# Kernel tuning notes

Measured on AMD Instinct MI355X. Metric: run time of the kernel, lower is better.

Reference implementation:

```python
import jax, jax.numpy as jnp
import numpy as np

B, S, E = 2, 2048, 1024
H, KVH, D = 16, 4, 64
ROPE_BASE = 10000.0


def setup_inputs() -> dict:
    key = jax.random.key(0)
    ks = jax.random.split(key, 7)
    s = 0.02
    return {
        "query_inputs": jax.random.normal(ks[0], (B, S, E), jnp.float32),
        "key_inputs": jax.random.normal(ks[1], (B, S, E), jnp.float32),
        "value_inputs": jax.random.normal(ks[2], (B, S, E), jnp.float32),
        "attention_mask": jnp.ones((1, 1, S, S), dtype=bool),
        "Wq": jax.random.normal(ks[3], (E, H * D), jnp.float32) * s,
        "Wk": jax.random.normal(ks[4], (E, KVH * D), jnp.float32) * s,
        "Wv": jax.random.normal(ks[5], (E, KVH * D), jnp.float32) * s,
        "Wo": jax.random.normal(ks[6], (H * D, E), jnp.float32) * s,
    }


def _rotate_half(x):
    x1, x2 = jnp.split(x, 2, axis=-1)
    return jnp.concatenate((-x2, x1), axis=-1)


def _rope(k, q):
    # standard RoPE, rescaling_factor=None -> base 10000
    d = q.shape[-1]
    inv_freq = 1.0 / (ROPE_BASE ** (jnp.arange(0, d, 2, dtype=jnp.float32) / d))
    t = jnp.arange(q.shape[1], dtype=jnp.float32)
    freqs = jnp.einsum("i,j->ij", t, inv_freq)          # [S, d/2]
    emb = jnp.concatenate((freqs, freqs), axis=-1)       # [S, d]
    cos = jnp.cos(emb)[None, :, None, :]                 # [1, S, 1, d]
    sin = jnp.sin(emb)[None, :, None, :]
    apply = lambda x: x * cos + _rotate_half(x) * sin
    return apply(k), apply(q)


def reference(query_inputs, key_inputs, value_inputs, attention_mask, Wq, Wk, Wv, Wo):
    q = (query_inputs @ Wq).reshape(B, S, H, D)
    k = (key_inputs @ Wk).reshape(B, S, KVH, D)
    v = (value_inputs @ Wv).reshape(B, S, KVH, D)
    k, q = _rope(k, q)
    n_rep = H // KVH
    k = jnp.repeat(k, n_rep, axis=2)                     # [B, S, H, D]
    v = jnp.repeat(v, n_rep, axis=2)
    logits = jnp.einsum("bthd,bThd->bhtT", q, k) / jnp.sqrt(jnp.float32(D))
    logits = jnp.where(attention_mask, logits, jnp.float32(-1e30))
    w = jax.nn.softmax(logits, axis=-1)                  # [B, H, S, S]
    out = jnp.einsum("bhtT,bThd->bthd", w, v).reshape(B, S, H * D)
    return out @ Wo
```

## Files before the change

kernel.cpp:

```cpp
#include <hip/hip_runtime.h>
#include <hip/hip_bf16.h>
#include <math.h>

#define Bsz 2
#define Sseq 2048
#define Edim 1024
#define Hq 16
#define KVH 4
#define Dh 64

typedef __attribute__((ext_vector_type(4))) float f32x4;
typedef __attribute__((ext_vector_type(16))) float f32x16;
typedef __attribute__((ext_vector_type(8))) short bf16x8;

__device__ inline unsigned short f2bf(float f) {
    union { float f; unsigned int u; } v; v.f = f;
    unsigned int u = v.u;
    u += 0x7FFFu + ((u >> 16) & 1u);
    return (unsigned short)(u >> 16);
}

__device__ inline unsigned int cvt_pk_bf16(float a, float b) {
    unsigned int r;
    asm("v_cvt_pk_bf16_f32 %0, %1, %2" : "=v"(r) : "v"(a), "v"(b));
    return r;
}

__device__ inline f32x4 mfma16(bf16x8 a, bf16x8 b, f32x4 c) {
    return __builtin_amdgcn_mfma_f32_16x16x32_bf16(a, b, c, 0, 0, 0);
}

__device__ inline f32x16 mfma32(bf16x8 a, bf16x8 b, f32x16 c) {
    return __builtin_amdgcn_mfma_f32_32x32x16_bf16(a, b, c, 0, 0, 0);
}

__device__ inline void gload_lds16(const void* g, void* l) {
    __builtin_amdgcn_global_load_lds(
        (const __attribute__((address_space(1))) unsigned int*)g,
        (__attribute__((address_space(3))) unsigned int*)l, 16, 0, 0);
}

__global__ __launch_bounds__(256)
void prep(const float* __restrict__ Xq, const float* __restrict__ Xk,
          const float* __restrict__ Xv,
          const float* __restrict__ Wq, const float* __restrict__ Wk,
          const float* __restrict__ Wv, const float* __restrict__ Wo,
          unsigned short* __restrict__ Xq_b, unsigned short* __restrict__ Xk_b,
          unsigned short* __restrict__ Xv_b,
          unsigned short* __restrict__ Wq_t, unsigned short* __restrict__ Wk_t,
          unsigned short* __restrict__ Wv_t, unsigned short* __restrict__ Wo_t,
          float* __restrict__ tab) {
    int bid = blockIdx.x;
    if (bid < 256) {
        int idx = bid * 256 + threadIdx.x;
        int s = idx >> 5, j = idx & 31;
        double inv = pow(10000.0, -(double)(2 * j) / 64.0);
        double a = (double)s * inv;
        tab[idx * 2 + 0] = (float)cos(a);
        tab[idx * 2 + 1] = (float)sin(a);
        return;
    }
    bid -= 256;
    if (bid < 12288) {
        const float* X; unsigned short* Y;
        if (bid < 4096)      { X = Xq; Y = Xq_b; }
        else if (bid < 8192) { X = Xk; Y = Xk_b; bid -= 4096; }
        else                 { X = Xv; Y = Xv_b; bid -= 8192; }
        int i = bid * 256 + threadIdx.x;
        float4 v = ((const float4*)X)[i];
        ushort4 o;
        o.x = f2bf(v.x); o.y = f2bf(v.y); o.z = f2bf(v.z); o.w = f2bf(v.w);
        ((ushort4*)Y)[i] = o;
        return;
    }
    bid -= 12288;
    const float* W; unsigned short* Wt; int N; int local;
    if (bid < 1024)      { W = Wq; Wt = Wq_t; N = 1024; local = bid; }
    else if (bid < 1280) { W = Wk; Wt = Wk_t; N = 256;  local = bid - 1024; }
    else if (bid < 1536) { W = Wv; Wt = Wv_t; N = 256;  local = bid - 1280; }
    else                 { W = Wo; Wt = Wo_t; N = 1024; local = bid - 1536; }
    __shared__ float tile[32][33];
    int nb = N >> 5;
    int bn = (local % nb) * 32, bk = (local / nb) * 32;
    int tx = threadIdx.x & 31, ty = threadIdx.x >> 5;
    #pragma unroll
    for (int i = 0; i < 32; i += 8)
        tile[ty + i][tx] = W[(size_t)(bk + ty + i) * N + bn + tx];
    __syncthreads();
    #pragma unroll
    for (int i = 0; i < 32; i += 8)
        Wt[(size_t)(bn + ty + i) * 1024 + bk + tx] = f2bf(tile[tx][ty + i]);
}

__global__ __launch_bounds__(256)
void qkv_gemm(const unsigned short* __restrict__ Xq_b,
              const unsigned short* __restrict__ Xk_b,
              const unsigned short* __restrict__ Xv_b,
              const unsigned short* __restrict__ Wq_t,
              const unsigned short* __restrict__ Wk_t,
              const unsigned short* __restrict__ Wv_t,
              unsigned short* __restrict__ Qb,
              unsigned short* __restrict__ Kbf,
              unsigned short* __restrict__ Vt,
              const float* __restrict__ tab, float qscale) {
    __shared__ __attribute__((aligned(16))) unsigned short Alds[128 * 64];
    __shared__ __attribute__((aligned(16))) unsigned short Blds[128 * 64];

    int bid = blockIdx.x;
    const unsigned short *A, *Bt;
    unsigned short* C;
    int m0, n0, N, epi;
    float prescale;
    if (bid < 256) {
        A = Xq_b; Bt = Wq_t; C = Qb;
        m0 = (bid & 31) << 7; n0 = (bid >> 5) << 7; N = 1024; epi = 0; prescale = qscale;
    } else if (bid < 320) {
        int l = bid - 256;
        A = Xk_b; Bt = Wk_t; C = Kbf;
        m0 = (l & 31) << 7; n0 = (l >> 5) << 7; N = 256; epi = 0; prescale = 1.f;
    } else {
        int l = bid - 320;
        A = Xv_b; Bt = Wv_t; C = Vt;
        m0 = (l & 31) << 7; n0 = (l >> 5) << 7; N = 256; epi = 1; prescale = 1.f;
    }

    const int t = threadIdx.x;
    const int wid = t >> 6, lane = t & 63;
    const int l15 = lane & 15, l4 = lane >> 4;
    const int wm = (wid >> 1) * 64, wn = (wid & 1) * 64;

    f32x4 acc[4][4] = {};

    for (int k0 = 0; k0 < 1024; k0 += 64) {
        #pragma unroll
        for (int i = 0; i < 4; ++i) {
            int slot = t + 256 * i;
            int row = slot >> 3, ch = slot & 7;
            int g = ch ^ (row & 7);
            gload_lds16(A + (size_t)(m0 + row) * 1024 + k0 + g * 8, &Alds[slot * 8]);
            gload_lds16(Bt + (size_t)(n0 + row) * 1024 + k0 + g * 8, &Blds[slot * 8]);
        }
        __syncthreads();
        __builtin_amdgcn_s_setprio(1);
        #pragma unroll
        for (int kc = 0; kc < 2; ++kc) {
            bf16x8 af[4], bfr[4];
            #pragma unroll
            for (int mt = 0; mt < 4; ++mt)
                af[mt] = *(const bf16x8*)&Alds[(wm + mt * 16 + l15) * 64 + (((kc * 4 + l4) ^ (l15 & 7)) * 8)];
            #pragma unroll
            for (int nt = 0; nt < 4; ++nt)
                bfr[nt] = *(const bf16x8*)&Blds[(wn + nt * 16 + l15) * 64 + (((kc * 4 + l4) ^ (l15 & 7)) * 8)];
            #pragma unroll
            for (int mt = 0; mt < 4; ++mt)
                #pragma unroll
                for (int nt = 0; nt < 4; ++nt)
                    acc[mt][nt] = mfma16(af[mt], bfr[nt], acc[mt][nt]);
        }
        __builtin_amdgcn_s_setprio(0);
        __syncthreads();
    }

    if (epi == 0) {
        #pragma unroll
        for (int mt = 0; mt < 4; ++mt) {
            int rbase = m0 + wm + mt * 16 + 4 * l4;
            #pragma unroll
            for (int nt = 0; nt < 2; ++nt) {
                int col = n0 + wn + nt * 16 + l15;
                int j = col & 31;
                #pragma unroll
                for (int r = 0; r < 4; ++r) {
                    int row = rbase + r;
                    int s = row & (Sseq - 1);
                    float c = tab[(s * 32 + j) * 2 + 0];
                    float sn = tab[(s * 32 + j) * 2 + 1];
                    float x1 = acc[mt][nt][r] * prescale;
                    float x2 = acc[mt][nt + 2][r] * prescale;
                    C[(size_t)row * N + col]      = f2bf(x1 * c - x2 * sn);
                    C[(size_t)row * N + col + 32] = f2bf(x2 * c + x1 * sn);
                }
            }
        }
    } else {
        #pragma unroll
        for (int mt = 0; mt < 4; ++mt)
            #pragma unroll
            for (int nt = 0; nt < 4; ++nt)
                #pragma unroll
                for (int r = 0; r < 4; ++r) {
                    int row = m0 + wm + mt * 16 + 4 * l4 + r;
                    int col = n0 + wn + nt * 16 + l15;
                    int b = row >> 11, s = row & (Sseq - 1);
                    C[((size_t)(b * 256 + col) << 11) + s] = f2bf(acc[mt][nt][r]);
                }
    }
}

__global__ __launch_bounds__(256)
void wo_gemm(const unsigned short* __restrict__ A,
             const unsigned short* __restrict__ Bt,
             float* __restrict__ C) {
    __shared__ __attribute__((aligned(16))) unsigned short Alds[128 * 64];
    __shared__ __attribute__((aligned(16))) unsigned short Blds[128 * 64];
    const int t = threadIdx.x;
    const int wid = t >> 6, lane = t & 63;
    const int l15 = lane & 15, l4 = lane >> 4;
    const int m0 = blockIdx.x * 128, n0 = blockIdx.y * 128;
    const int wm = (wid >> 1) * 64, wn = (wid & 1) * 64;

    f32x4 acc[4][4] = {};

    for (int k0 = 0; k0 < 1024; k0 += 64) {
        #pragma unroll
        for (int i = 0; i < 4; ++i) {
            int slot = t + 256 * i;
            int row = slot >> 3, ch = slot & 7;
            int g = ch ^ (row & 7);
            gload_lds16(A + (size_t)(m0 + row) * 1024 + k0 + g * 8, &Alds[slot * 8]);
            gload_lds16(Bt + (size_t)(n0 + row) * 1024 + k0 + g * 8, &Blds[slot * 8]);
        }
        __syncthreads();
        __builtin_amdgcn_s_setprio(1);
        #pragma unroll
        for (int kc = 0; kc < 2; ++kc) {
            bf16x8 af[4], bfr[4];
            #pragma unroll
            for (int mt = 0; mt < 4; ++mt)
                af[mt] = *(const bf16x8*)&Alds[(wm + mt * 16 + l15) * 64 + (((kc * 4 + l4) ^ (l15 & 7)) * 8)];
            #pragma unroll
            for (int nt = 0; nt < 4; ++nt)
                bfr[nt] = *(const bf16x8*)&Blds[(wn + nt * 16 + l15) * 64 + (((kc * 4 + l4) ^ (l15 & 7)) * 8)];
            #pragma unroll
            for (int mt = 0; mt < 4; ++mt)
                #pragma unroll
                for (int nt = 0; nt < 4; ++nt)
                    acc[mt][nt] = mfma16(af[mt], bfr[nt], acc[mt][nt]);
        }
        __builtin_amdgcn_s_setprio(0);
        __syncthreads();
    }

    #pragma unroll
    for (int mt = 0; mt < 4; ++mt)
        #pragma unroll
        for (int nt = 0; nt < 4; ++nt)
            #pragma unroll
            for (int r = 0; r < 4; ++r)
                C[(size_t)(m0 + wm + mt * 16 + 4 * l4 + r) * 1024 + n0 + wn + nt * 16 + l15]
                    = acc[mt][nt][r];
}

__global__ __launch_bounds__(128)
void attn(const unsigned short* __restrict__ Q,
          const unsigned short* __restrict__ Kb,
          const unsigned short* __restrict__ Vt,
          unsigned short* __restrict__ O) {
    __shared__ __attribute__((aligned(16))) unsigned short Klds[2][64 * 64];
    __shared__ __attribute__((aligned(16))) unsigned short Vlds[2][64 * 64];

    const int t = threadIdx.x, wid = t >> 6, lane = t & 63;
    const int l31 = lane & 31, hi = lane >> 5;
    const int q0 = blockIdx.x * 64;
    const int bh = blockIdx.y;
    const int b = bh >> 4, h = bh & 15, kvh = h >> 2;
    const int qb0 = (b << 11) + q0 + wid * 32;

    bf16x8 qf[4];
    {
        const unsigned short* qp = Q + (size_t)(qb0 + l31) * 1024 + h * 64 + hi * 8;
        #pragma unroll
        for (int kc = 0; kc < 4; ++kc)
            qf[kc] = *(const bf16x8*)(qp + kc * 16);
    }

    f32x16 accO[2] = {};
    float lrow = 0.f;

    #define STAGE(buf, kt)                                                              \
        do {                                                                            \
            int kbase = (kt) * 64;                                                      \
            _Pragma("unroll")                                                           \
            for (int i = 0; i < 4; ++i) {                                               \
                int slot = t + 128 * i;                                                 \
                int row = slot >> 3, ch = slot & 7;                                     \
                int g = ch ^ (row & 7);                                                 \
                gload_lds16(Kb + ((size_t)((b << 11) + kbase + row) << 8) + kvh * 64 + g * 8, \
                            &Klds[buf][slot * 8]);                                      \
                gload_lds16(Vt + ((size_t)((b * 4 + kvh) * 64 + row) << 11) + kbase + g * 8,  \
                            &Vlds[buf][slot * 8]);                                      \
            }                                                                           \
        } while (0)

    STAGE(0, 0);
    asm volatile("s_waitcnt vmcnt(0)");
    __syncthreads();

    int cur = 0;
    for (int kt = 0; kt < Sseq / 64; ++kt) {
        if (kt + 1 < Sseq / 64) STAGE(cur ^ 1, kt + 1);

        f32x16 sacc[2] = {};
        __builtin_amdgcn_s_setprio(1);
        #pragma unroll
        for (int kc = 0; kc < 4; ++kc) {
            #pragma unroll
            for (int kb = 0; kb < 2; ++kb) {
                int row = kb * 32 + l31;
                bf16x8 kf = *(const bf16x8*)
                    &Klds[cur][row * 64 + (((kc * 2 + hi) ^ (row & 7)) * 8)];
                sacc[kb] = mfma32(kf, qf[kc], sacc[kb]);
            }
        }
        __builtin_amdgcn_s_setprio(0);

        float pv[2][16];
        float rs = 0.f;
        #pragma unroll
        for (int kb = 0; kb < 2; ++kb)
            #pragma unroll
            for (int r = 0; r < 16; ++r) {
                float p = __builtin_amdgcn_exp2f(sacc[kb][r]);
                pv[kb][r] = p;
                rs += p;
            }
        lrow += rs + __shfl_xor(rs, 32);

        bf16x8 pa[4];
        #pragma unroll
        for (int kb = 0; kb < 2; ++kb) {
            #pragma unroll
            for (int half = 0; half < 2; ++half) {
                const float* p = &pv[kb][half * 8];
                unsigned int u0 = cvt_pk_bf16(p[0], p[1]);
                unsigned int u1 = cvt_pk_bf16(p[2], p[3]);
                unsigned int u2 = cvt_pk_bf16(p[4], p[5]);
                unsigned int u3 = cvt_pk_bf16(p[6], p[7]);
                asm("v_permlane32_swap_b32 %0, %1" : "+v"(u0), "+v"(u2));
                asm("v_permlane32_swap_b32 %0, %1" : "+v"(u1), "+v"(u3));
                uint4 w; w.x = u0; w.y = u1; w.z = u2; w.w = u3;
                pa[kb * 2 + half] = *(bf16x8*)&w;
            }
        }

        __builtin_amdgcn_s_setprio(1);
        #pragma unroll
        for (int kq = 0; kq < 4; ++kq) {
            #pragma unroll
            for (int db = 0; db < 2; ++db) {
                int row = db * 32 + l31;
                bf16x8 vf = *(const bf16x8*)
                    &Vlds[cur][row * 64 + (((kq * 2 + hi) ^ (row & 7)) * 8)];
                accO[db] = mfma32(pa[kq], vf, accO[db]);
            }
        }
        __builtin_amdgcn_s_setprio(0);

        asm volatile("s_waitcnt vmcnt(0)");
        __syncthreads();
        cur ^= 1;
    }
    #undef STAGE

    float linv = __builtin_amdgcn_rcpf(lrow);
    #pragma unroll
    for (int r = 0; r < 16; ++r) {
        int q = (r & 3) + 8 * (r >> 2) + 4 * hi;
        float li = __shfl(linv, q);
        #pragma unroll
        for (int db = 0; db < 2; ++db) {
            int col = h * 64 + db * 32 + l31;
            O[(size_t)(qb0 + q) * 1024 + col] = f2bf(accO[db][r] * li);
        }
    }
}

extern "C" void kernel_launch(void* const* d_in, const int* in_sizes, int n_in,
                              void* d_out, int out_size, void* d_ws, size_t ws_size,
                              hipStream_t stream) {
    const float* Xq = (const float*)d_in[0];
    const float* Xk = (const float*)d_in[1];
    const float* Xv = (const float*)d_in[2];
    const float* Wq = (const float*)d_in[4];
    const float* Wk = (const float*)d_in[5];
    const float* Wv = (const float*)d_in[6];
    const float* Wo = (const float*)d_in[7];

    char* ws = (char*)d_ws;
    unsigned short* Xq_b = (unsigned short*)(ws + 0);
    unsigned short* Xk_b = (unsigned short*)(ws + 8388608);
    unsigned short* Xv_b = (unsigned short*)(ws + 16777216);
    unsigned short* Qb   = (unsigned short*)(ws + 25165824);
    unsigned short* Kbf  = (unsigned short*)(ws + 33554432);
    unsigned short* Vt   = (unsigned short*)(ws + 35651584);
    unsigned short* AttO = (unsigned short*)(ws + 37748736);
    unsigned short* Wq_t = (unsigned short*)(ws + 46137344);
    unsigned short* Wk_t = (unsigned short*)(ws + 48234496);
    unsigned short* Wv_t = (unsigned short*)(ws + 48758784);
    unsigned short* Wo_t = (unsigned short*)(ws + 49283072);
    float*          tab  = (float*)(ws + 51380224);

    prep<<<dim3(15104), 256, 0, stream>>>(Xq, Xk, Xv, Wq, Wk, Wv, Wo,
                                          Xq_b, Xk_b, Xv_b,
                                          Wq_t, Wk_t, Wv_t, Wo_t, tab);

    const float qscale = 0.125f * 1.44269504088896340736f;
    qkv_gemm<<<dim3(384), 256, 0, stream>>>(Xq_b, Xk_b, Xv_b, Wq_t, Wk_t, Wv_t,
                                            Qb, Kbf, Vt, tab, qscale);

    attn<<<dim3(32, 32), 128, 0, stream>>>(Qb, Kbf, Vt, AttO);

    wo_gemm<<<dim3(32, 8), 256, 0, stream>>>(AttO, Wo_t, (float*)d_out);
}
```

Baseline: 115.9 us.

## Split attention over key halves with separate combine kernel

The attention kernel now uses 256-thread blocks covering 128 queries and splits the key sequence into two halves across grid z, writing unnormalized-per-half outputs and row sums to workspace. A new combine kernel reweights the two partial outputs by their row sums and writes the final bf16 attention output. This doubles the grid size and shares each K/V tile between four waves, trading an extra kernel launch, extra global traffic for the partial results, and an added bf16 rounding step. The unnormalized exp without max subtraction already relies on bounded logits, and the combine keeps that approach.

```diff
diff --git a/kernel.cpp b/kernel.cpp
--- a/kernel.cpp
+++ b/kernel.cpp
@@ -18,6 +18,11 @@
     unsigned int u = v.u;
     u += 0x7FFFu + ((u >> 16) & 1u);
     return (unsigned short)(u >> 16);
+}
+
+__device__ inline float bf2f(unsigned short u) {
+    union { unsigned int u; float f; } v; v.u = (unsigned int)u << 16;
+    return v.f;
 }
 
 __device__ inline unsigned int cvt_pk_bf16(float a, float b) {
@@ -251,20 +256,23 @@
                     = acc[mt][nt][r];
 }
 
-__global__ __launch_bounds__(128)
-void attn(const unsigned short* __restrict__ Q,
-          const unsigned short* __restrict__ Kb,
-          const unsigned short* __restrict__ Vt,
-          unsigned short* __restrict__ O) {
+__global__ __launch_bounds__(256, 4)
+void attn_split(const unsigned short* __restrict__ Q,
+                const unsigned short* __restrict__ Kb,
+                const unsigned short* __restrict__ Vt,
+                unsigned short* __restrict__ Op,
+                float* __restrict__ Lp) {
     __shared__ __attribute__((aligned(16))) unsigned short Klds[2][64 * 64];
     __shared__ __attribute__((aligned(16))) unsigned short Vlds[2][64 * 64];
 
     const int t = threadIdx.x, wid = t >> 6, lane = t & 63;
     const int l31 = lane & 31, hi = lane >> 5;
-    const int q0 = blockIdx.x * 64;
+    const int q0 = blockIdx.x * 128;
     const int bh = blockIdx.y;
+    const int half = blockIdx.z;
     const int b = bh >> 4, h = bh & 15, kvh = h >> 2;
     const int qb0 = (b << 11) + q0 + wid * 32;
+    const int kh0 = half * 1024;
 
     bf16x8 qf[4];
     {
@@ -279,10 +287,10 @@
 
     #define STAGE(buf, kt)                                                              \
         do {                                                                            \
-            int kbase = (kt) * 64;                                                      \
+            int kbase = kh0 + (kt) * 64;                                                \
             _Pragma("unroll")                                                           \
-            for (int i = 0; i < 4; ++i) {                                               \
-                int slot = t + 128 * i;                                                 \
+            for (int i = 0; i < 2; ++i) {                                               \
+                int slot = t + 256 * i;                                                 \
                 int row = slot >> 3, ch = slot & 7;                                     \
                 int g = ch ^ (row & 7);                                                 \
                 gload_lds16(Kb + ((size_t)((b << 11) + kbase + row) << 8) + kvh * 64 + g * 8, \
@@ -297,8 +305,8 @@
     __syncthreads();
 
     int cur = 0;
-    for (int kt = 0; kt < Sseq / 64; ++kt) {
-        if (kt + 1 < Sseq / 64) STAGE(cur ^ 1, kt + 1);
+    for (int kt = 0; kt < 16; ++kt) {
+        if (kt + 1 < 16) STAGE(cur ^ 1, kt + 1);
 
         f32x16 sacc[2] = {};
         __builtin_amdgcn_s_setprio(1);
@@ -330,8 +338,8 @@
         #pragma unroll
         for (int kb = 0; kb < 2; ++kb) {
             #pragma unroll
-            for (int half = 0; half < 2; ++half) {
-                const float* p = &pv[kb][half * 8];
+            for (int hf = 0; hf < 2; ++hf) {
+                const float* p = &pv[kb][hf * 8];
                 unsigned int u0 = cvt_pk_bf16(p[0], p[1]);
                 unsigned int u1 = cvt_pk_bf16(p[2], p[3]);
                 unsigned int u2 = cvt_pk_bf16(p[4], p[5]);
@@ -339,7 +347,7 @@
                 asm("v_permlane32_swap_b32 %0, %1" : "+v"(u0), "+v"(u2));
                 asm("v_permlane32_swap_b32 %0, %1" : "+v"(u1), "+v"(u3));
                 uint4 w; w.x = u0; w.y = u1; w.z = u2; w.w = u3;
-                pa[kb * 2 + half] = *(bf16x8*)&w;
+                pa[kb * 2 + hf] = *(bf16x8*)&w;
             }
         }
 
@@ -363,16 +371,38 @@
     #undef STAGE
 
     float linv = __builtin_amdgcn_rcpf(lrow);
+    unsigned short* Oh = Op + (size_t)half * 4194304;
     #pragma unroll
     for (int r = 0; r < 16; ++r) {
         int q = (r & 3) + 8 * (r >> 2) + 4 * hi;
         float li = __shfl(linv, q);
         #pragma unroll
-        for (int db = 0; db < 2; ++db) {
-            int col = h * 64 + db * 32 + l31;
-            O[(size_t)(qb0 + q) * 1024 + col] = f2bf(accO[db][r] * li);
-        }
-    }
+        for (int db = 0; db < 2; ++db)
+            Oh[(size_t)(qb0 + q) * 1024 + h * 64 + db * 32 + l31] = f2bf(accO[db][r] * li);
+    }
+    if (hi == 0)
+        Lp[half * 65536 + (bh << 11) + q0 + wid * 32 + l31] = lrow;
+}
+
+__global__ __launch_bounds__(256)
+void combine(const unsigned short* __restrict__ Op, const float* __restrict__ Lp,
+             unsigned short* __restrict__ AttO) {
+    const int q = blockIdx.x, t = threadIdx.x;
+    const int b = q >> 11, s = q & 2047, h = t >> 4;
+    const int bh = (b << 4) | h;
+    float l0 = Lp[(bh << 11) + s];
+    float l1 = Lp[65536 + (bh << 11) + s];
+    float w = __builtin_amdgcn_rcpf(l0 + l1);
+    float w0 = l0 * w, w1 = l1 * w;
+    size_t idx = (size_t)q * 1024 + t * 4;
+    ushort4 a = *(const ushort4*)(Op + idx);
+    ushort4 c = *(const ushort4*)(Op + 4194304 + idx);
+    ushort4 o;
+    o.x = f2bf(w0 * bf2f(a.x) + w1 * bf2f(c.x));
+    o.y = f2bf(w0 * bf2f(a.y) + w1 * bf2f(c.y));
+    o.z = f2bf(w0 * bf2f(a.z) + w1 * bf2f(c.z));
+    o.w = f2bf(w0 * bf2f(a.w) + w1 * bf2f(c.w));
+    *(ushort4*)(AttO + idx) = o;
 }
 
 extern "C" void kernel_launch(void* const* d_in, const int* in_sizes, int n_in,
@@ -399,6 +429,8 @@
     unsigned short* Wv_t = (unsigned short*)(ws + 48758784);
     unsigned short* Wo_t = (unsigned short*)(ws + 49283072);
     float*          tab  = (float*)(ws + 51380224);
+    unsigned short* Op   = (unsigned short*)(ws + 0);
+    float*          Lp   = (float*)(ws + 16777216);
 
     prep<<<dim3(15104), 256, 0, stream>>>(Xq, Xk, Xv, Wq, Wk, Wv, Wo,
                                           Xq_b, Xk_b, Xv_b,
@@ -408,7 +440,8 @@
     qkv_gemm<<<dim3(384), 256, 0, stream>>>(Xq_b, Xk_b, Xv_b, Wq_t, Wk_t, Wv_t,
                                             Qb, Kbf, Vt, tab, qscale);
 
-    attn<<<dim3(32, 32), 128, 0, stream>>>(Qb, Kbf, Vt, AttO);
+    attn_split<<<dim3(16, 32, 2), 256, 0, stream>>>(Qb, Kbf, Vt, Op, Lp);
+    combine<<<dim3(4096), 256, 0, stream>>>(Op, Lp, AttO);
 
     wo_gemm<<<dim3(32, 8), 256, 0, stream>>>(AttO, Wo_t, (float*)d_out);
 }
```

Measured after the change: 112.4 us. 3.1% less time.
